# Kernel tuning notes

Measured on AMD Instinct MI355X. Metric: run time of the kernel, lower is better.

The kernel has to match this reference:

```python
import jax, jax.numpy as jnp
import numpy as np

N_NODES = 50000
N_EDGES = 800000
D = 128
H = 4  # num_heads
LN_EPS = 1e-5


def setup_inputs() -> dict:
    key = jax.random.key(0)
    ks = jax.random.split(key, 6)
    x = jax.random.normal(ks[0], (N_NODES, D), jnp.float32)
    edge_index0 = jax.random.randint(ks[1], (2, N_EDGES), 0, N_NODES, dtype=jnp.int32)
    edge_index1 = jax.random.randint(ks[2], (2, N_EDGES), 0, N_NODES, dtype=jnp.int32)
    s = 1.0 / np.sqrt(D)
    w_in = jax.random.uniform(ks[3], (3 * D, D), jnp.float32, -s, s)   # packed q,k,v proj
    b_in = jnp.zeros((3 * D,), jnp.float32)
    w_out = jax.random.uniform(ks[4], (D, D), jnp.float32, -s, s)
    b_out = jnp.zeros((D,), jnp.float32)
    ln_gamma = jnp.ones((D,), jnp.float32)
    ln_beta = jnp.zeros((D,), jnp.float32)
    return {"x": x, "edge_index0": edge_index0, "edge_index1": edge_index1,
            "w_in": w_in, "b_in": b_in, "w_out": w_out, "b_out": b_out,
            "ln_gamma": ln_gamma, "ln_beta": ln_beta}


def _multi_agg(x, edge_index, n):
    """Scatter multi-reduce (max/min/sum/mean). Returns [n, 4, d], zeros for isolated nodes."""
    src, dst = edge_index[0], edge_index[1]
    msgs = x[src]                                                    # [E, d] gather
    cnt = jax.ops.segment_sum(jnp.ones((msgs.shape[0],), msgs.dtype), dst, num_segments=n)
    has = (cnt > 0)[:, None]
    ssum = jax.ops.segment_sum(msgs, dst, num_segments=n)
    smax = jnp.where(has, jax.ops.segment_max(msgs, dst, num_segments=n), 0.0)
    smin = jnp.where(has, jax.ops.segment_min(msgs, dst, num_segments=n), 0.0)
    smean = ssum / jnp.maximum(cnt, 1.0)[:, None]
    return jnp.stack([smax, smin, ssum, smean], axis=1)             # [n, 4, d]


def reference(x, edge_index0, edge_index1, w_in, b_in, w_out, b_out, ln_gamma, ln_beta):
    n, d = x.shape
    dh = d // H
    a0 = _multi_agg(x, edge_index0, n)                               # [n, 4, d]
    a1 = _multi_agg(x, edge_index1, n)
    aggr = jnp.concatenate([a0, a1], axis=1)                         # [n, 8, d]
    tokens = jnp.concatenate([x[:, None, :], aggr], axis=1)         # [n, S=9, d]
    S = tokens.shape[1]
    # key padding mask: self token never masked; aggr tokens masked where all-zero
    mask = jnp.concatenate([jnp.zeros((n, 1), bool),
                            jnp.all(aggr == 0, axis=2)], axis=1)    # [n, S]
    # multihead self-attention (eval mode, no dropout)
    qw, kw, vw = jnp.split(w_in, 3, axis=0)
    qb, kb, vb = jnp.split(b_in, 3)
    q = (tokens @ qw.T + qb).reshape(n, S, H, dh)
    k = (tokens @ kw.T + kb).reshape(n, S, H, dh)
    v = (tokens @ vw.T + vb).reshape(n, S, H, dh)
    scores = jnp.einsum('nshd,nthd->nhst', q, k) / np.sqrt(dh)      # [n, H, S, S]
    scores = jnp.where(mask[:, None, None, :], -1e30, scores)
    attn = jax.nn.softmax(scores, axis=-1)
    o = jnp.einsum('nhst,nthd->nshd', attn, v).reshape(n, S, d)
    o = o @ w_out.T + b_out
    self_out = o[:, 0, :]                                            # [n, d]
    # LayerNorm
    mu = jnp.mean(self_out, axis=-1, keepdims=True)
    var = jnp.var(self_out, axis=-1, keepdims=True)
    return (self_out - mu) * jax.lax.rsqrt(var + LN_EPS) * ln_gamma + ln_beta
```

## Files before the change

### kernel.cpp

```cpp
#include <hip/hip_runtime.h>
#include <hip/hip_fp16.h>
#include <math.h>

#define NNODES 50000
#define NEDGES 800000
#define D 128
#define NPB 8
#define TROWS 72
#define TS 136
#define OS 132
#define CAP 64
#define NBINS 196
#define BSTRIDE 4608
#define EPB1 4096
#define P1PS ((NEDGES + EPB1 - 1) / EPB1)
#define WSWZ_SLOTS 2048
#define WKT_BASE 2048
#define WO_BASE 4096
#define B2_BASE 12288
#define X16_BASE 12416
#define PREP_SLOTS (X16_BASE + NNODES * D / 4)
#define PREP_BLOCKS ((PREP_SLOTS + 255) / 256)

typedef _Float16 half_t;
typedef half_t half2v __attribute__((ext_vector_type(2)));
typedef half_t half4 __attribute__((ext_vector_type(4)));
typedef half_t half8 __attribute__((ext_vector_type(8)));
typedef float floatx4 __attribute__((ext_vector_type(4)));
typedef unsigned short ushort_t;



__global__ __launch_bounds__(256) void prep1_kernel(
    const int* __restrict__ ei0, const int* __restrict__ ei1,
    int* __restrict__ cursor, unsigned int* __restrict__ arena,
    const float* __restrict__ w_in, const float* __restrict__ w_out,
    const float* __restrict__ b_in, const float* __restrict__ b_out,
    const float* __restrict__ x,
    half_t* __restrict__ w_swz, half_t* __restrict__ wkT_swz,
    half_t* __restrict__ wo_swz,
    float* __restrict__ b2, half_t* __restrict__ x16) {
  const int t = threadIdx.x;
  const int b = blockIdx.x;
  if (b < 2 * P1PS) {
    __shared__ int hist[256], cur[256], baseA[256];
    const int set = (b >= P1PS);
    const int blk = set ? (b - P1PS) : b;
    const int* ei = set ? ei1 : ei0;
    hist[t] = 0; cur[t] = 0;
    __syncthreads();
    int dd[16], ss[16];
#pragma unroll
    for (int g = 0; g < 4; ++g) {
      int e = blk * EPB1 + g * 1024 + t * 4;
      if (e < NEDGES) {
        int4 dv = *(const int4*)(ei + NEDGES + e);
        int4 sv = *(const int4*)(ei + e);
        dd[g * 4 + 0] = dv.x; dd[g * 4 + 1] = dv.y;
        dd[g * 4 + 2] = dv.z; dd[g * 4 + 3] = dv.w;
        ss[g * 4 + 0] = sv.x; ss[g * 4 + 1] = sv.y;
        ss[g * 4 + 2] = sv.z; ss[g * 4 + 3] = sv.w;
      } else {
        dd[g * 4 + 0] = -1; dd[g * 4 + 1] = -1; dd[g * 4 + 2] = -1; dd[g * 4 + 3] = -1;
        ss[g * 4 + 0] = 0;  ss[g * 4 + 1] = 0;  ss[g * 4 + 2] = 0;  ss[g * 4 + 3] = 0;
      }
    }
#pragma unroll
    for (int i = 0; i < 16; ++i)
      if (dd[i] >= 0) atomicAdd(&hist[dd[i] >> 8], 1);
    __syncthreads();
    if (t < NBINS) {
      int h = hist[t];
      baseA[t] = h ? atomicAdd(&cursor[set * NBINS + t], h) : 0;
    }
    __syncthreads();
#pragma unroll
    for (int i = 0; i < 16; ++i) {
      if (dd[i] >= 0) {
        int bin = dd[i] >> 8;
        int pos = atomicAdd(&cur[bin], 1) + baseA[bin];
        if (pos < BSTRIDE)
          arena[(size_t)(set * NBINS + bin) * BSTRIDE + pos] =
              ((unsigned)(dd[i] & 255) << 16) | (unsigned)ss[i];
      }
    }
    return;
  }
  int slot = (b - 2 * P1PS) * 256 + t;
  if (slot < WSWZ_SLOTS) {
    int c = slot >> 6, l = slot & 63;
    int nt = c >> 2, ks = c & 3;
    int n = nt * 16 + (l & 15);
    int kb = ks * 32 + (l >> 4) * 8;
    half_t* dst = w_swz + (size_t)slot * 8;
#pragma unroll
    for (int j = 0; j < 8; ++j) dst[j] = (half_t)w_in[n * 128 + kb + j];
  } else if (slot < WO_BASE) {
    int s2 = slot - WKT_BASE;
    int c2 = s2 >> 6, l = s2 & 63;
    int mt = c2 >> 2, h = c2 & 3;
    int m = mt * 16 + (l & 15);
    int j0 = (l >> 4) * 8;
    half_t* dst = wkT_swz + (size_t)s2 * 8;
#pragma unroll
    for (int j = 0; j < 8; ++j)
      dst[j] = (half_t)w_in[(size_t)(128 + h * 32 + j0 + j) * 128 + m];
  } else if (slot < B2_BASE) {
    int s2 = slot - WO_BASE;
    int c2 = s2 >> 6, l = s2 & 63;
    int nt = c2 >> 4, ksc = c2 & 15;
    int n = nt * 16 + (l & 15);
    int h = ksc >> 2;
    int kb = (ksc & 3) * 32 + (l >> 4) * 8;
    float acc[8] = {0.f, 0.f, 0.f, 0.f, 0.f, 0.f, 0.f, 0.f};
    for (int jj = 0; jj < 32; ++jj) {
      float wo = w_out[n * 128 + h * 32 + jj];
      const float* wr = w_in + (size_t)(256 + h * 32 + jj) * 128 + kb;
#pragma unroll
      for (int j = 0; j < 8; ++j) acc[j] = fmaf(wo, wr[j], acc[j]);
    }
    half_t* dst = wo_swz + (size_t)s2 * 8;
#pragma unroll
    for (int j = 0; j < 8; ++j) dst[j] = (half_t)acc[j];
  } else if (slot < X16_BASE) {
    int i = slot - B2_BASE;
    float acc = b_out[i];
    for (int j = 0; j < 128; ++j) acc = fmaf(w_out[i * 128 + j], b_in[256 + j], acc);
    b2[i] = acc;
  } else {
    int idx = slot - X16_BASE;
    if (idx < NNODES * D / 4) {
      float4 v = ((const float4*)x)[idx];
      union { half_t h[4]; uint2 u64; } p;
      p.h[0] = (half_t)v.x; p.h[1] = (half_t)v.y;
      p.h[2] = (half_t)v.z; p.h[3] = (half_t)v.w;
      ((uint2*)x16)[idx] = p.u64;
    }
  }
}


__global__ __launch_bounds__(256) void prep2_kernel(
    const int* __restrict__ cursor, const unsigned int* __restrict__ arena,
    int* __restrict__ cnt0, int* __restrict__ cnt1,
    ushort_t* __restrict__ A0, ushort_t* __restrict__ A1) {
  __shared__ int cntL[256];
  const int t = threadIdx.x;
  const int b = blockIdx.x;
  int set = (b >= NBINS);
  int bin = set ? (b - NBINS) : b;
  cntL[t] = 0;
  __syncthreads();
  int T = cursor[set * NBINS + bin];
  T = T > BSTRIDE ? BSTRIDE : T;
  ushort_t* A = set ? A1 : A0;
  int* cnt = set ? cnt1 : cnt0;
  const unsigned* arn = arena + (size_t)(set * NBINS + bin) * BSTRIDE;
  for (int i = t; i < T; i += 256) {
    unsigned rec = arn[i];
    int r = (rec >> 16) & 0xFF;
    int pos = atomicAdd(&cntL[r], 1);
    if (pos < CAP)
      A[(size_t)(bin * 256 + r) * CAP + pos] = (ushort_t)(rec & 0xFFFF);
  }
  __syncthreads();
  int idx = bin * 256 + t;
  if (idx < NNODES) cnt[idx] = cntL[t] > CAP ? CAP : cntL[t];
}


__global__ __launch_bounds__(512, 8) void fused_attn_kernel(
    const half_t* __restrict__ x16,
    const int* __restrict__ cnt0, const ushort_t* __restrict__ A0,
    const int* __restrict__ cnt1, const ushort_t* __restrict__ A1,
    const half_t* __restrict__ w_swz, const half_t* __restrict__ wkT_swz,
    const half_t* __restrict__ wo_swz,
    const float* __restrict__ b_in, const float* __restrict__ b2,
    const float* __restrict__ gamma, const float* __restrict__ beta,
    float* __restrict__ out) {
  __shared__ half_t tokS[TROWS * TS];
  __shared__ half_t qS[8 * TS];
  __shared__ half_t yzS[32 * TS];
  __shared__ float scS[NPB][4][9];
  __shared__ int cntS[NPB][2];

  const int tid = threadIdx.x;
  const int lane = tid & 63, wv = tid >> 6;
  const int quad = lane >> 4, l15 = lane & 15;
  const int slot = quad;
  const int d16 = l15;
  const int node = blockIdx.x * NPB + wv;
  const int node_s = __builtin_amdgcn_readfirstlane(node);

  int c0 = cnt0[node_s];
  int c1 = cnt1[node_s];
  if (lane == 0) { cntS[wv][0] = c0; cntS[wv][1] = c1; }
  int ent0 = A0[(size_t)node_s * CAP + lane];
  int ent1 = A1[(size_t)node_s * CAP + lane];
  uint selfw = ((const uint*)(x16 + (size_t)node * 128))[lane];

  {
    half2v mxA[4], mnA[4], mxB[4], mnB[4];
    float sA[8], sB[8];
    const half_t NINF = (half_t)(-INFINITY), PINF = (half_t)INFINITY;
#pragma unroll
    for (int p = 0; p < 4; ++p) {
      mxA[p] = (half2v){NINF, NINF}; mnA[p] = (half2v){PINF, PINF};
      mxB[p] = (half2v){NINF, NINF}; mnB[p] = (half2v){PINF, PINF};
    }
#pragma unroll
    for (int e = 0; e < 8; ++e) { sA[e] = 0.f; sB[e] = 0.f; }

    auto issue4 = [&](int entv, int c, int j, uint4* rv) {
#pragma unroll
      for (int u = 0; u < 4; ++u) {
        int r = j + u * 4 + slot;
        int rc = (r < c) ? r : (c - 1);
        int src = __shfl(entv, rc);
        rv[u] = *(const uint4*)(x16 + (size_t)src * 128 + d16 * 8);
      }
    };
    auto accum4 = [&](const uint4* rv, int j, int c, half2v* mx2, half2v* mn2,
                      float* sum) {
      half2v ps[4] = {(half2v){(half_t)0, (half_t)0}, (half2v){(half_t)0, (half_t)0},
                      (half2v){(half_t)0, (half_t)0}, (half2v){(half_t)0, (half_t)0}};
#pragma unroll
      for (int u = 0; u < 4; ++u) {
        int r = j + u * 4 + slot;
        if (r < c) {
          union { uint4 q; half2v p2[4]; } cc;
          cc.q = rv[u];
#pragma unroll
          for (int p = 0; p < 4; ++p) {
            mx2[p] = __builtin_elementwise_max(mx2[p], cc.p2[p]);
            mn2[p] = __builtin_elementwise_min(mn2[p], cc.p2[p]);
            ps[p] = ps[p] + cc.p2[p];
          }
        }
      }
#pragma unroll
      for (int p = 0; p < 4; ++p) {
        sum[2 * p] += (float)ps[p][0];
        sum[2 * p + 1] += (float)ps[p][1];
      }
    };

    uint4 rva[4], rvb[4];
    if (c0 > 0) issue4(ent0, c0, 0, rva);
    if (c1 > 0) issue4(ent1, c1, 0, rvb);
    if (c0 > 0) accum4(rva, 0, c0, mxA, mnA, sA);
    if (c1 > 0) accum4(rvb, 0, c1, mxB, mnB, sB);
    for (int j = 16; j < c0; j += 16) { issue4(ent0, c0, j, rva); accum4(rva, j, c0, mxA, mnA, sA); }
    for (int j = 16; j < c1; j += 16) { issue4(ent1, c1, j, rvb); accum4(rvb, j, c1, mxB, mnB, sB); }

    union HB { half2v h; int i; };
    auto finish = [&](int c, half2v* mx2, half2v* mn2, float* sum, int set) {
#pragma unroll
      for (int p = 0; p < 4; ++p) {
        HB a, b;
        a.h = mx2[p];
        b.i = __shfl_xor(a.i, 16); a.h = __builtin_elementwise_max(a.h, b.h);
        b.i = __shfl_xor(a.i, 32); a.h = __builtin_elementwise_max(a.h, b.h);
        mx2[p] = a.h;
        a.h = mn2[p];
        b.i = __shfl_xor(a.i, 16); a.h = __builtin_elementwise_min(a.h, b.h);
        b.i = __shfl_xor(a.i, 32); a.h = __builtin_elementwise_min(a.h, b.h);
        mn2[p] = a.h;
      }
#pragma unroll
      for (int e = 0; e < 8; ++e) {
        sum[e] += __shfl_xor(sum[e], 16);
        sum[e] += __shfl_xor(sum[e], 32);
      }
      float inv = 1.f / (float)(c > 1 ? c : 1);
      union { uint4 q; half2v p2[4]; half_t h[8]; } o;
      if (slot == 0) {
#pragma unroll
        for (int p = 0; p < 4; ++p) o.p2[p] = mx2[p];
      } else if (slot == 1) {
#pragma unroll
        for (int p = 0; p < 4; ++p) o.p2[p] = mn2[p];
      } else if (slot == 2) {
#pragma unroll
        for (int e = 0; e < 8; ++e) o.h[e] = (half_t)sum[e];
      } else {
#pragma unroll
        for (int e = 0; e < 8; ++e) o.h[e] = (half_t)(sum[e] * inv);
      }
      if (c == 0) o.q = make_uint4(0, 0, 0, 0);
      *(uint4*)(tokS + (size_t)(8 + wv * 8 + 4 * set + slot) * TS + d16 * 8) = o.q;
    };
    finish(c0, mxA, mnA, sA, 0);
    finish(c1, mxB, mnB, sB, 1);

    ((uint*)(tokS + wv * TS))[lane] = selfw;
  }
  __syncthreads();

  {
    int nt = wv;
    half8 aw[4];
#pragma unroll
    for (int ks = 0; ks < 4; ++ks)
      aw[ks] = *(const half8*)(w_swz + ((size_t)(nt * 4 + ks) * 64 + lane) * 8);
    int col0 = nt * 16 + quad * 4;
    float4 bias = *(const float4*)(b_in + col0);
    floatx4 acc = {0.f, 0.f, 0.f, 0.f};
#pragma unroll
    for (int ks = 0; ks < 4; ++ks) {
      half8 tb = *(const half8*)(tokS + l15 * TS + ks * 32 + quad * 8);
      acc = __builtin_amdgcn_mfma_f32_16x16x32_f16(aw[ks], tb, acc, 0, 0, 0);
    }
    if (l15 < 8) {
      half4 hv = {(half_t)(acc[0] + bias.x), (half_t)(acc[1] + bias.y),
                  (half_t)(acc[2] + bias.z), (half_t)(acc[3] + bias.w)};
      *(half4*)(qS + l15 * TS + col0) = hv;
    }
  }
  __syncthreads();

  {
    int col0 = wv * 16 + quad * 4;
    int qr = l15 & 7;
#pragma unroll
    for (int h = 0; h < 4; ++h) {
      half8 awk = *(const half8*)(wkT_swz + ((size_t)(wv * 4 + h) * 64 + lane) * 8);
      half8 qb = *(const half8*)(qS + qr * TS + h * 32 + quad * 8);
      floatx4 acc = {0.f, 0.f, 0.f, 0.f};
      acc = __builtin_amdgcn_mfma_f32_16x16x32_f16(awk, qb, acc, 0, 0, 0);
      if (l15 < 8) {
        half4 hv = {(half_t)acc[0], (half_t)acc[1], (half_t)acc[2], (half_t)acc[3]};
        *(half4*)(yzS + (l15 * 4 + h) * TS + col0) = hv;
      }
    }
  }
  __syncthreads();

  {
    int t = l15;
    int trow = (t == 0) ? wv : ((t <= 8) ? (8 + wv * 8 + (t - 1)) : wv);
    int yrow = wv * 4 + (l15 & 3);
    floatx4 acc = {0.f, 0.f, 0.f, 0.f};
#pragma unroll
    for (int ks = 0; ks < 4; ++ks) {
      half8 av = *(const half8*)(yzS + yrow * TS + ks * 32 + quad * 8);
      half8 bv = *(const half8*)(tokS + trow * TS + ks * 32 + quad * 8);
      acc = __builtin_amdgcn_mfma_f32_16x16x32_f16(av, bv, acc, 0, 0, 0);
    }
    if (quad == 0 && t < 9) {
      bool masked = (t >= 1) && (cntS[wv][(t - 1) >> 2] == 0);
#pragma unroll
      for (int h = 0; h < 4; ++h)
        scS[wv][h][t] = masked ? -1e30f : acc[h] * 0.17677669529663687f;
    }
  }

  if (lane < 4) {
    int h = lane;
    float m = -INFINITY;
#pragma unroll
    for (int t = 0; t < 9; ++t) m = fmaxf(m, scS[wv][h][t]);
    float ev[9], sum = 0.f;
#pragma unroll
    for (int t = 0; t < 9; ++t) { ev[t] = __expf(scS[wv][h][t] - m); sum += ev[t]; }
    float inv = 1.f / sum;
#pragma unroll
    for (int t = 0; t < 9; ++t) scS[wv][h][t] = ev[t] * inv;
  }

  {
    float za[4] = {0.f, 0.f, 0.f, 0.f}, zb[4] = {0.f, 0.f, 0.f, 0.f};
#pragma unroll
    for (int t = 0; t < 9; ++t) {
      int trow = (t == 0) ? wv : (8 + wv * 8 + (t - 1));
      half2v tv = *(const half2v*)(tokS + trow * TS + 2 * lane);
      float t0 = (float)tv[0], t1 = (float)tv[1];
#pragma unroll
      for (int h = 0; h < 4; ++h) {
        float a = scS[wv][h][t];
        za[h] = fmaf(a, t0, za[h]);
        zb[h] = fmaf(a, t1, zb[h]);
      }
    }
#pragma unroll
    for (int h = 0; h < 4; ++h) {
      half2v zv = {(half_t)za[h], (half_t)zb[h]};
      *(half2v*)(yzS + (wv * 4 + h) * TS + 2 * lane) = zv;
    }
  }
  __syncthreads();

  float* oo = (float*)tokS;
  {
    floatx4 acc = {0.f, 0.f, 0.f, 0.f};
#pragma unroll
    for (int hp = 0; hp < 2; ++hp) {
      half8 awb[8];
#pragma unroll
      for (int i = 0; i < 8; ++i)
        awb[i] = *(const half8*)(wo_swz + ((size_t)(wv * 16 + hp * 8 + i) * 64 + lane) * 8);
#pragma unroll
      for (int i = 0; i < 8; ++i) {
        int ksc = hp * 8 + i;
        int h = ksc >> 2;
        int zr = (l15 < 8) ? (l15 * 4 + h) : h;
        half8 ob = *(const half8*)(yzS + zr * TS + (ksc & 3) * 32 + quad * 8);
        acc = __builtin_amdgcn_mfma_f32_16x16x32_f16(awb[i], ob, acc, 0, 0, 0);
      }
    }
    if (l15 < 8) {
      int col0 = wv * 16 + quad * 4;
      float4 bias = *(const float4*)(b2 + col0);
      float4 r;
      r.x = acc[0] + bias.x; r.y = acc[1] + bias.y;
      r.z = acc[2] + bias.z; r.w = acc[3] + bias.w;
      *(float4*)(oo + l15 * OS + col0) = r;
    }
  }
  __syncthreads();

  {
    float v[2];
    float sum = 0.f, sq = 0.f;
#pragma unroll
    for (int u = 0; u < 2; ++u) {
      int c = lane + 64 * u;
      v[u] = oo[wv * OS + c];
      sum += v[u];
      sq += v[u] * v[u];
    }
#pragma unroll
    for (int m = 1; m < 64; m <<= 1) {
      sum += __shfl_xor(sum, m);
      sq += __shfl_xor(sq, m);
    }
    float mu = sum * (1.f / 128.f);
    float var = sq * (1.f / 128.f) - mu * mu;
    float rs = rsqrtf(var + 1e-5f);
#pragma unroll
    for (int u = 0; u < 2; ++u) {
      int c = lane + 64 * u;
      out[(size_t)node * 128 + c] = (v[u] - mu) * rs * gamma[c] + beta[c];
    }
  }
}


extern "C" void kernel_launch(void* const* d_in, const int* in_sizes, int n_in,
                              void* d_out, int out_size, void* d_ws, size_t ws_size,
                              hipStream_t stream) {
  const float* x = (const float*)d_in[0];
  const int* ei0 = (const int*)d_in[1];
  const int* ei1 = (const int*)d_in[2];
  const float* w_in = (const float*)d_in[3];
  const float* b_in = (const float*)d_in[4];
  const float* w_out = (const float*)d_in[5];
  const float* b_out = (const float*)d_in[6];
  const float* gamma = (const float*)d_in[7];
  const float* beta = (const float*)d_in[8];
  float* out = (float*)d_out;

  char* wsB = (char*)d_ws;
  size_t off = 0;
  int* cursor = (int*)(wsB + off);       off += ((size_t)2 * NBINS * 4 + 15) & ~(size_t)15;
  unsigned int* arena = (unsigned int*)(wsB + off);
  off += (size_t)2 * NBINS * BSTRIDE * 4;
  int* cnt0 = (int*)(wsB + off); off += (size_t)NNODES * 4;
  int* cnt1 = (int*)(wsB + off); off += (size_t)NNODES * 4;
  ushort_t* A0 = (ushort_t*)(wsB + off); off += (size_t)NNODES * CAP * 2;
  ushort_t* A1 = (ushort_t*)(wsB + off); off += (size_t)NNODES * CAP * 2;
  off = (off + 15) & ~(size_t)15;
  half_t* w_swz = (half_t*)(wsB + off);   off += (size_t)WSWZ_SLOTS * 8 * 2;
  half_t* wkT_swz = (half_t*)(wsB + off); off += (size_t)2048 * 8 * 2;
  half_t* wo_swz = (half_t*)(wsB + off);  off += (size_t)8192 * 8 * 2;
  float* b2 = (float*)(wsB + off);        off += 128 * sizeof(float);
  half_t* x16 = (half_t*)(wsB + off);     off += (size_t)NNODES * 128 * 2;

  hipMemsetAsync(cursor, 0, 2 * NBINS * sizeof(int), stream);

  prep1_kernel<<<2 * P1PS + PREP_BLOCKS, 256, 0, stream>>>(
      ei0, ei1, cursor, arena, w_in, w_out, b_in, b_out, x,
      w_swz, wkT_swz, wo_swz, b2, x16);
  prep2_kernel<<<2 * NBINS, 256, 0, stream>>>(cursor, arena, cnt0, cnt1, A0, A1);
  fused_attn_kernel<<<NNODES / NPB, 512, 0, stream>>>(x16, cnt0, A0, cnt1, A1,
                                                      w_swz, wkT_swz, wo_swz,
                                                      b_in, b2, gamma, beta, out);
}
```

Baseline: 237.5 us.

## Locally sort edge records in LDS before coalesced bin writes; shrink out-proj prefetch batch

The edge binning pass now counting-sorts each block's edges by bin in shared memory, using a prefix scan over the histogram. It then writes the records to the global arena in contiguous runs per bin instead of scattering each edge individually, which is meant to improve write coalescing. The output-projection loop also prefetches 4 weight fragments per step instead of 8, lowering register pressure. The costs are an extra 16KB of LDS, a serial 8-step scan with barriers, and less load-ahead in the projection loop.

```diff
diff --git a/kernel.cpp b/kernel.cpp
--- a/kernel.cpp
+++ b/kernel.cpp
@@ -43,46 +43,65 @@
   const int t = threadIdx.x;
   const int b = blockIdx.x;
   if (b < 2 * P1PS) {
-    __shared__ int hist[256], cur[256], baseA[256];
+    __shared__ int hist[256], scan[256], cur[256], baseA[256];
+    __shared__ unsigned recS[EPB1];
     const int set = (b >= P1PS);
     const int blk = set ? (b - P1PS) : b;
     const int* ei = set ? ei1 : ei0;
-    hist[t] = 0; cur[t] = 0;
+    hist[t] = 0;
     __syncthreads();
-    int dd[16], ss[16];
+    int bins[16];
+    unsigned recs[16];
 #pragma unroll
     for (int g = 0; g < 4; ++g) {
       int e = blk * EPB1 + g * 1024 + t * 4;
       if (e < NEDGES) {
         int4 dv = *(const int4*)(ei + NEDGES + e);
         int4 sv = *(const int4*)(ei + e);
-        dd[g * 4 + 0] = dv.x; dd[g * 4 + 1] = dv.y;
-        dd[g * 4 + 2] = dv.z; dd[g * 4 + 3] = dv.w;
-        ss[g * 4 + 0] = sv.x; ss[g * 4 + 1] = sv.y;
-        ss[g * 4 + 2] = sv.z; ss[g * 4 + 3] = sv.w;
+        int dd[4] = {dv.x, dv.y, dv.z, dv.w};
+        int ss[4] = {sv.x, sv.y, sv.z, sv.w};
+#pragma unroll
+        for (int u = 0; u < 4; ++u) {
+          bins[g * 4 + u] = dd[u] >> 8;
+          recs[g * 4 + u] = ((unsigned)(dd[u] & 255) << 16) | (unsigned)ss[u];
+        }
       } else {
-        dd[g * 4 + 0] = -1; dd[g * 4 + 1] = -1; dd[g * 4 + 2] = -1; dd[g * 4 + 3] = -1;
-        ss[g * 4 + 0] = 0;  ss[g * 4 + 1] = 0;  ss[g * 4 + 2] = 0;  ss[g * 4 + 3] = 0;
+#pragma unroll
+        for (int u = 0; u < 4; ++u) { bins[g * 4 + u] = -1; recs[g * 4 + u] = 0; }
       }
     }
 #pragma unroll
     for (int i = 0; i < 16; ++i)
-      if (dd[i] >= 0) atomicAdd(&hist[dd[i] >> 8], 1);
+      if (bins[i] >= 0) atomicAdd(&hist[bins[i]], 1);
     __syncthreads();
-    if (t < NBINS) {
-      int h = hist[t];
-      baseA[t] = h ? atomicAdd(&cursor[set * NBINS + t], h) : 0;
-    }
+    int v = hist[t];
+    scan[t] = v;
     __syncthreads();
+    for (int off = 1; off < 256; off <<= 1) {
+      int y = (t >= off) ? scan[t - off] : 0;
+      __syncthreads();
+      scan[t] += y;
+      __syncthreads();
+    }
+    if (t < NBINS && v > 0) baseA[t] = atomicAdd(&cursor[set * NBINS + t], v);
+    else baseA[t] = 0;
+    cur[t] = scan[t] - v;
+    __syncthreads();
 #pragma unroll
     for (int i = 0; i < 16; ++i) {
-      if (dd[i] >= 0) {
-        int bin = dd[i] >> 8;
-        int pos = atomicAdd(&cur[bin], 1) + baseA[bin];
-        if (pos < BSTRIDE)
-          arena[(size_t)(set * NBINS + bin) * BSTRIDE + pos] =
-              ((unsigned)(dd[i] & 255) << 16) | (unsigned)ss[i];
-      }
+      if (bins[i] >= 0) {
+        int p = atomicAdd(&cur[bins[i]], 1);
+        recS[p] = ((unsigned)bins[i] << 24) | recs[i];
+      }
+    }
+    __syncthreads();
+    int tot = scan[255];
+    for (int i = t; i < tot; i += 256) {
+      unsigned r = recS[i];
+      int bn = r >> 24;
+      int ofs = baseA[bn] + (i - (scan[bn] - hist[bn]));
+      if (ofs < BSTRIDE)
+        arena[(size_t)(set * NBINS + bn) * BSTRIDE + ofs] = r & 0xFFFFFF;
     }
     return;
   }
@@ -394,14 +413,14 @@
   {
     floatx4 acc = {0.f, 0.f, 0.f, 0.f};
 #pragma unroll
-    for (int hp = 0; hp < 2; ++hp) {
-      half8 awb[8];
-#pragma unroll
-      for (int i = 0; i < 8; ++i)
-        awb[i] = *(const half8*)(wo_swz + ((size_t)(wv * 16 + hp * 8 + i) * 64 + lane) * 8);
-#pragma unroll
-      for (int i = 0; i < 8; ++i) {
-        int ksc = hp * 8 + i;
+    for (int hp = 0; hp < 4; ++hp) {
+      half8 awb[4];
+#pragma unroll
+      for (int i = 0; i < 4; ++i)
+        awb[i] = *(const half8*)(wo_swz + ((size_t)(wv * 16 + hp * 4 + i) * 64 + lane) * 8);
+#pragma unroll
+      for (int i = 0; i < 4; ++i) {
+        int ksc = hp * 4 + i;
         int h = ksc >> 2;
         int zr = (l15 < 8) ? (l15 * 4 + h) : h;
         half8 ob = *(const half8*)(yzS + zr * TS + (ksc & 3) * 32 + quad * 8);
```

Result: faster. 232.8 us (-2.0%).
